# Optimization experiments

Measured on AMD Instinct MI355X. Metric: run time of the kernel, lower is better.

The kernel has to match this reference:

```python
import jax, jax.numpy as jnp
import numpy as np

BATCH = 131072
STATE_DIM = 64
CONTROL_DIM = 16
HIDDEN = 256
ALPHA = 0.1
MAX_ITERS = 200
TOL = 0.01
TRACKED_ITERS = 5
U_MIN, U_MAX = -1.0, 1.0


def setup_inputs() -> dict:
    key = jax.random.key(0)
    ks = jax.random.split(key, 8)
    def w(k, shape, fan_in):
        return (jax.random.normal(k, shape, jnp.float32) / np.float32(np.sqrt(fan_in)))
    x = jax.random.normal(ks[0], (BATCH, STATE_DIM), jnp.float32)
    t = jax.random.uniform(ks[1], (1,), jnp.float32)
    W1 = w(ks[2], (STATE_DIM + 1, HIDDEN), STATE_DIM + 1)
    b1 = jnp.zeros((HIDDEN,), jnp.float32)
    W2 = w(ks[3], (HIDDEN, HIDDEN), HIDDEN)
    b2 = jnp.zeros((HIDDEN,), jnp.float32)
    W3 = w(ks[4], (HIDDEN, STATE_DIM), HIDDEN)
    b3 = jnp.zeros((STATE_DIM,), jnp.float32)
    Bmat = w(ks[5], (STATE_DIM, CONTROL_DIM), STATE_DIM)  # oc_problem dynamics matrix
    return {"x": x, "t": t, "W1": W1, "b1": b1, "W2": W2, "b2": b2,
            "W3": W3, "b3": b3, "Bmat": Bmat}


def _p_net(t, x, W1, b1, W2, b2, W3, b3):
    # DefaultPNet: pad x with scalar t, then 3-layer ReLU MLP -> p in [B, state_dim]
    n = x.shape[0]
    tcol = jnp.broadcast_to(t.reshape(1, 1).astype(x.dtype), (n, 1))
    zt = jnp.concatenate([x, tcol], axis=1)
    h = jax.nn.relu(zt @ W1 + b1)
    h = jax.nn.relu(h @ W2 + b2)
    return h @ W3 + b3


def reference(x, t, W1, b1, W2, b2, W3, b3, Bmat):
    # grad_H_u(t,x,u,p) = u + p @ Bmat  (LQ Hamiltonian); p independent of u,
    # so p is computed once (same math as recomputing it every iteration).
    p = _p_net(t, x, W1, b1, W2, b2, W3, b3)          # [B, state_dim]
    pB = p @ Bmat                                      # [B, control_dim]
    clamp = lambda u: jnp.clip(u, U_MIN, U_MAX)
    T = lambda u, pb: u - ALPHA * (u + pb)

    u0 = jnp.zeros((x.shape[0], CONTROL_DIM), x.dtype)
    pB_ng = jax.lax.stop_gradient(pB)

    def cond(st):
        _, i, res = st
        return (res >= TOL) & (i < MAX_ITERS)

    def body(st):
        u, i, _ = st
        u_new = clamp(T(u, pB_ng))
        res = jnp.max(jnp.linalg.norm(u_new - u, axis=1)) / ALPHA
        return (u_new, i + 1, res)

    u_fp, _, _ = jax.lax.while_loop(cond, body, (u0, jnp.int32(0), jnp.float32(jnp.inf)))

    # training path: tracked_iters differentiable refinement steps + final T
    u = jax.lax.stop_gradient(u_fp)
    for _ in range(TRACKED_ITERS + 1):
        u = clamp(T(u, pB))
    return u
```

## Files before the change

kernel.cpp:

```cpp
#include <hip/hip_runtime.h>


typedef __bf16 bf16;
typedef __bf16 bf16x8 __attribute__((ext_vector_type(8)));
typedef __bf16 bf16x4 __attribute__((ext_vector_type(4)));
typedef float  f32x4  __attribute__((ext_vector_type(4)));

#define HID    256
#define SDIM   64
#define CDIM   16
#define BM     128
#define NTILES 1024
#define GRID   256
#define LDH    264
#define LDX    72

#define OFF_W1P 0
#define OFF_W2P 32768
#define OFF_W3P 163840

#define MFMA(a, b, c) __builtin_amdgcn_mfma_f32_16x16x32_bf16(a, b, c, 0, 0, 0)

__global__ __launch_bounds__(256)
void oc_setup(const float* __restrict__ W1, const float* __restrict__ W2,
              const float* __restrict__ W3, const float* __restrict__ Bmat,
              char* __restrict__ ws) {
  const int gid = blockIdx.x * 256 + threadIdx.x;
  if (gid < 2048) {
    const int f = gid, lane = f & 63, tt = f >> 6;
    const int nt = tt & 15, kt = tt >> 4;
    const int col = nt * 16 + (lane & 15);
    const int krow = kt * 32 + ((lane >> 4) << 3);
    bf16x8 v;
#pragma unroll
    for (int j = 0; j < 8; ++j) v[j] = (bf16)W1[(krow + j) * HID + col];
    *(bf16x8*)((bf16*)(ws + OFF_W1P) + (size_t)f * 8) = v;
  } else if (gid < 10240) {
    const int f = gid - 2048, lane = f & 63, tt = f >> 6;
    const int nt = tt & 15, kt = tt >> 4;
    const int col = nt * 16 + (lane & 15);
    const int krow = kt * 32 + ((lane >> 4) << 3);
    bf16x8 v;
#pragma unroll
    for (int j = 0; j < 8; ++j) v[j] = (bf16)W2[(krow + j) * HID + col];
    *(bf16x8*)((bf16*)(ws + OFF_W2P) + (size_t)f * 8) = v;
  } else if (gid < 10752) {
    const int f = gid - 10240, lane = f & 63, kt = f >> 6;
    const int lrow = lane & 15;
    const int krow = kt * 32 + ((lane >> 4) << 3);
    bf16x8 v;
#pragma unroll
    for (int j = 0; j < 8; ++j) {
      float s = 0.f;
      for (int m = 0; m < SDIM; ++m)
        s = fmaf(W3[(krow + j) * SDIM + m], Bmat[m * CDIM + lrow], s);
      v[j] = (bf16)s;
    }
    *(bf16x8*)((bf16*)(ws + OFF_W3P) + (size_t)f * 8) = v;
  }
}

__global__ __launch_bounds__(512, 2)
void oc_main(const float* __restrict__ x,  const float* __restrict__ t,
             const float* __restrict__ W1, const float* __restrict__ b1,
             const float* __restrict__ b2g, const float* __restrict__ b3,
             const float* __restrict__ Bmat, const char* __restrict__ ws,
             float* __restrict__ out) {
  __shared__ bf16 sH1[BM][LDH];
  __shared__ bf16 sH2[BM][LDH];
  __shared__ bf16 sX [BM][LDX];
  const int tid  = threadIdx.x;
  const int wave = tid >> 6, lane = tid & 63;
  const int quad = lane >> 4, lrow = lane & 15;

  const bf16* W1p = (const bf16*)(ws + OFF_W1P);
  const bf16* W2p = (const bf16*)(ws + OFF_W2P);
  const bf16* W3p = (const bf16*)(ws + OFF_W3P);

  bf16x8 B1[2][2], B2[8][2];
#pragma unroll
  for (int kt = 0; kt < 2; ++kt)
#pragma unroll
    for (int j = 0; j < 2; ++j)
      B1[kt][j] = *(const bf16x8*)(W1p + ((size_t)(kt * 16 + 2 * wave + j) * 64 + lane) * 8);
#pragma unroll
  for (int kt = 0; kt < 8; ++kt)
#pragma unroll
    for (int j = 0; j < 2; ++j)
      B2[kt][j] = *(const bf16x8*)(W2p + ((size_t)(kt * 16 + 2 * wave + j) * 64 + lane) * 8);

  const float tt = t[0];
  float b1e[2], b2r[2];
#pragma unroll
  for (int j = 0; j < 2; ++j) {
    const int c = (2 * wave + j) * 16 + lrow;
    b1e[j] = b1[c] + tt * W1[SDIM * HID + c];
    b2r[j] = b2g[c];
  }
  float b3B = 0.f;
  for (int m = 0; m < SDIM; ++m) b3B = fmaf(b3[m], Bmat[m * CDIM + lrow], b3B);

  auto stage = [&](int tile) {
    const float* xp = x + (size_t)tile * BM * SDIM;
#pragma unroll
    for (int i = 0; i < 4; ++i) {
      const int q = i * 512 + tid;
      const int r = q >> 4, k4 = (q & 15) * 4;
      const float4 v = *(const float4*)(xp + r * SDIM + k4);
      bf16x4 w = {(bf16)v.x, (bf16)v.y, (bf16)v.z, (bf16)v.w};
      *(bf16x4*)(&sX[r][k4]) = w;
    }
  };

  f32x4 acc[8][2];
  int tile = blockIdx.x;
  stage(tile);
  __syncthreads();

  while (true) {
#pragma unroll
    for (int mt = 0; mt < 8; ++mt) {
      acc[mt][0] = (f32x4){0.f, 0.f, 0.f, 0.f};
      acc[mt][1] = (f32x4){0.f, 0.f, 0.f, 0.f};
    }
#pragma unroll
    for (int kt = 0; kt < 2; ++kt)
#pragma unroll
      for (int mt = 0; mt < 8; ++mt) {
        const bf16x8 a = *(const bf16x8*)(&sX[mt * 16 + lrow][kt * 32 + quad * 8]);
        acc[mt][0] = MFMA(a, B1[kt][0], acc[mt][0]);
        acc[mt][1] = MFMA(a, B1[kt][1], acc[mt][1]);
      }
#pragma unroll
    for (int j = 0; j < 2; ++j) {
      const int c = (2 * wave + j) * 16 + lrow;
#pragma unroll
      for (int mt = 0; mt < 8; ++mt)
#pragma unroll
        for (int r = 0; r < 4; ++r)
          sH1[mt * 16 + quad * 4 + r][c] = (bf16)fmaxf(acc[mt][j][r] + b1e[j], 0.f);
    }
    __syncthreads();

#pragma unroll
    for (int mt = 0; mt < 8; ++mt) {
      acc[mt][0] = (f32x4){0.f, 0.f, 0.f, 0.f};
      acc[mt][1] = (f32x4){0.f, 0.f, 0.f, 0.f};
    }
#pragma unroll
    for (int kt = 0; kt < 8; ++kt)
#pragma unroll
      for (int mt = 0; mt < 8; ++mt) {
        const bf16x8 a = *(const bf16x8*)(&sH1[mt * 16 + lrow][kt * 32 + quad * 8]);
        acc[mt][0] = MFMA(a, B2[kt][0], acc[mt][0]);
        acc[mt][1] = MFMA(a, B2[kt][1], acc[mt][1]);
      }
    const int next = tile + GRID;
    if (next < NTILES) stage(next);
    __syncthreads();

#pragma unroll
    for (int j = 0; j < 2; ++j) {
      const int c = (2 * wave + j) * 16 + lrow;
#pragma unroll
      for (int mt = 0; mt < 8; ++mt)
#pragma unroll
        for (int r = 0; r < 4; ++r) {
          const float v = fmaxf(acc[mt][j][r] + b2r[j], 0.f);
          const bf16 hi = (bf16)v;
          sH2[mt * 16 + quad * 4 + r][c] = hi;
          sH1[mt * 16 + quad * 4 + r][c] = (bf16)(v - (float)hi);
        }
    }
    __syncthreads();

    f32x4 a3 = (f32x4){0.f, 0.f, 0.f, 0.f};
#pragma unroll
    for (int kt = 0; kt < 8; ++kt) {
      const bf16x8 b  = *(const bf16x8*)(W3p + ((size_t)(kt * 64) + lane) * 8);
      const bf16x8 ah = *(const bf16x8*)(&sH2[16 * wave + lrow][kt * 32 + quad * 8]);
      const bf16x8 al = *(const bf16x8*)(&sH1[16 * wave + lrow][kt * 32 + quad * 8]);
      a3 = MFMA(ah, b, a3);
      a3 = MFMA(al, b, a3);
    }
    float* op = out + ((size_t)tile * BM + 16 * wave + quad * 4) * CDIM + lrow;
#pragma unroll
    for (int r = 0; r < 4; ++r)
      op[r * CDIM] = fminf(fmaxf(-(a3[r] + b3B), -1.f), 1.f);

    tile = next;
    if (tile >= NTILES) break;
    __syncthreads();
  }
}

extern "C" void kernel_launch(void* const* d_in, const int* in_sizes, int n_in,
                              void* d_out, int out_size, void* d_ws, size_t ws_size,
                              hipStream_t stream) {
  const float* x    = (const float*)d_in[0];
  const float* t    = (const float*)d_in[1];
  const float* W1   = (const float*)d_in[2];
  const float* b1   = (const float*)d_in[3];
  const float* W2   = (const float*)d_in[4];
  const float* b2   = (const float*)d_in[5];
  const float* W3   = (const float*)d_in[6];
  const float* b3   = (const float*)d_in[7];
  const float* Bmat = (const float*)d_in[8];
  float* out = (float*)d_out;
  char*  ws  = (char*)d_ws;

  hipLaunchKernelGGL(oc_setup, dim3(42), dim3(256), 0, stream, W1, W2, W3, Bmat, ws);
  hipLaunchKernelGGL(oc_main, dim3(GRID), dim3(512), 0, stream,
                     x, t, W1, b1, b2, b3, Bmat, ws, out);
}
```

Measured before the change: 130.7 us.

## Fuse weight prep into main kernel, transpose MFMA roles, swizzle shared memory

Drops the separate setup kernel and workspace. Each block now converts W1/W2 to bf16 fragments directly from global memory and computes W3·Bmat into shared memory. The GEMMs are transposed so weights are the A operand and activations the B operand, which allows vectorized bf16x4 stores of hidden activations and float4 output stores. An XOR swizzle on shared-memory hidden buffers reduces bank conflicts. The trade-off is redundant per-block weight conversion with strided, uncoalesced fp32 loads of W1/W2, in exchange for removing one kernel launch.

```diff
diff --git a/kernel.cpp b/kernel.cpp
--- a/kernel.cpp
+++ b/kernel.cpp
@@ -10,186 +10,192 @@
 #define SDIM   64
 #define CDIM   16
 #define BM     128
-#define NTILES 1024
 #define GRID   256
+#define ITERS  4
 #define LDH    264
 #define LDX    72
 
-#define OFF_W1P 0
-#define OFF_W2P 32768
-#define OFF_W3P 163840
-
 #define MFMA(a, b, c) __builtin_amdgcn_mfma_f32_16x16x32_bf16(a, b, c, 0, 0, 0)
 
-__global__ __launch_bounds__(256)
-void oc_setup(const float* __restrict__ W1, const float* __restrict__ W2,
-              const float* __restrict__ W3, const float* __restrict__ Bmat,
-              char* __restrict__ ws) {
-  const int gid = blockIdx.x * 256 + threadIdx.x;
-  if (gid < 2048) {
-    const int f = gid, lane = f & 63, tt = f >> 6;
-    const int nt = tt & 15, kt = tt >> 4;
-    const int col = nt * 16 + (lane & 15);
-    const int krow = kt * 32 + ((lane >> 4) << 3);
-    bf16x8 v;
-#pragma unroll
-    for (int j = 0; j < 8; ++j) v[j] = (bf16)W1[(krow + j) * HID + col];
-    *(bf16x8*)((bf16*)(ws + OFF_W1P) + (size_t)f * 8) = v;
-  } else if (gid < 10240) {
-    const int f = gid - 2048, lane = f & 63, tt = f >> 6;
-    const int nt = tt & 15, kt = tt >> 4;
-    const int col = nt * 16 + (lane & 15);
-    const int krow = kt * 32 + ((lane >> 4) << 3);
-    bf16x8 v;
-#pragma unroll
-    for (int j = 0; j < 8; ++j) v[j] = (bf16)W2[(krow + j) * HID + col];
-    *(bf16x8*)((bf16*)(ws + OFF_W2P) + (size_t)f * 8) = v;
-  } else if (gid < 10752) {
-    const int f = gid - 10240, lane = f & 63, kt = f >> 6;
-    const int lrow = lane & 15;
-    const int krow = kt * 32 + ((lane >> 4) << 3);
-    bf16x8 v;
-#pragma unroll
-    for (int j = 0; j < 8; ++j) {
-      float s = 0.f;
-      for (int m = 0; m < SDIM; ++m)
-        s = fmaf(W3[(krow + j) * SDIM + m], Bmat[m * CDIM + lrow], s);
-      v[j] = (bf16)s;
-    }
-    *(bf16x8*)((bf16*)(ws + OFF_W3P) + (size_t)f * 8) = v;
-  }
+__device__ __forceinline__ int sh_idx(int row, int h) {
+  const int g = (h >> 3) ^ (row & 7);
+  return row * LDH + g * 8 + (h & 7);
 }
 
 __global__ __launch_bounds__(512, 2)
 void oc_main(const float* __restrict__ x,  const float* __restrict__ t,
              const float* __restrict__ W1, const float* __restrict__ b1,
-             const float* __restrict__ b2g, const float* __restrict__ b3,
-             const float* __restrict__ Bmat, const char* __restrict__ ws,
-             float* __restrict__ out) {
-  __shared__ bf16 sH1[BM][LDH];
-  __shared__ bf16 sH2[BM][LDH];
-  __shared__ bf16 sX [BM][LDX];
+             const float* __restrict__ W2, const float* __restrict__ b2,
+             const float* __restrict__ W3, const float* __restrict__ b3,
+             const float* __restrict__ Bmat, float* __restrict__ out) {
+  __shared__ bf16 sH1[BM * LDH];
+  __shared__ bf16 sH2[BM * LDH];
+  __shared__ bf16 sX [BM * LDX];
   const int tid  = threadIdx.x;
   const int wave = tid >> 6, lane = tid & 63;
-  const int quad = lane >> 4, lrow = lane & 15;
-
-  const bf16* W1p = (const bf16*)(ws + OFF_W1P);
-  const bf16* W2p = (const bf16*)(ws + OFF_W2P);
-  const bf16* W3p = (const bf16*)(ws + OFF_W3P);
-
-  bf16x8 B1[2][2], B2[8][2];
-#pragma unroll
-  for (int kt = 0; kt < 2; ++kt)
-#pragma unroll
-    for (int j = 0; j < 2; ++j)
-      B1[kt][j] = *(const bf16x8*)(W1p + ((size_t)(kt * 16 + 2 * wave + j) * 64 + lane) * 8);
-#pragma unroll
-  for (int kt = 0; kt < 8; ++kt)
-#pragma unroll
-    for (int j = 0; j < 2; ++j)
-      B2[kt][j] = *(const bf16x8*)(W2p + ((size_t)(kt * 16 + 2 * wave + j) * 64 + lane) * 8);
-
-  const float tt = t[0];
-  float b1e[2], b2r[2];
-#pragma unroll
-  for (int j = 0; j < 2; ++j) {
-    const int c = (2 * wave + j) * 16 + lrow;
-    b1e[j] = b1[c] + tt * W1[SDIM * HID + c];
-    b2r[j] = b2g[c];
-  }
-  float b3B = 0.f;
-  for (int m = 0; m < SDIM; ++m) b3B = fmaf(b3[m], Bmat[m * CDIM + lrow], b3B);
+  const int q    = lane >> 4, l = lane & 15;
 
   auto stage = [&](int tile) {
     const float* xp = x + (size_t)tile * BM * SDIM;
 #pragma unroll
     for (int i = 0; i < 4; ++i) {
-      const int q = i * 512 + tid;
-      const int r = q >> 4, k4 = (q & 15) * 4;
+      const int e = i * 512 + tid;
+      const int r = e >> 4, k4 = (e & 15) * 4;
       const float4 v = *(const float4*)(xp + r * SDIM + k4);
       bf16x4 w = {(bf16)v.x, (bf16)v.y, (bf16)v.z, (bf16)v.w};
-      *(bf16x4*)(&sX[r][k4]) = w;
+      *(bf16x4*)(&sX[r * LDX + k4]) = w;
     }
   };
 
-  f32x4 acc[8][2];
-  int tile = blockIdx.x;
-  stage(tile);
+  {
+    const int n1 = tid >> 1;
+    const int cb = (tid & 1) * 8;
+    float aw[8];
+#pragma unroll
+    for (int i = 0; i < 8; ++i) aw[i] = 0.f;
+    for (int m = 0; m < SDIM; ++m) {
+      const float w = W3[n1 * SDIM + m];
+      const float4 bA = *(const float4*)(&Bmat[m * CDIM + cb]);
+      const float4 bB = *(const float4*)(&Bmat[m * CDIM + cb + 4]);
+      aw[0] = fmaf(w, bA.x, aw[0]); aw[1] = fmaf(w, bA.y, aw[1]);
+      aw[2] = fmaf(w, bA.z, aw[2]); aw[3] = fmaf(w, bA.w, aw[3]);
+      aw[4] = fmaf(w, bB.x, aw[4]); aw[5] = fmaf(w, bB.y, aw[5]);
+      aw[6] = fmaf(w, bB.z, aw[6]); aw[7] = fmaf(w, bB.w, aw[7]);
+    }
+    const int kt = n1 >> 5, qq = (n1 >> 3) & 3, jj = n1 & 7;
+#pragma unroll
+    for (int ci = 0; ci < 8; ++ci)
+      sH1[(kt * 64 + qq * 16 + cb + ci) * 8 + jj] = (bf16)aw[ci];
+  }
+  stage(blockIdx.x);
   __syncthreads();
 
-  while (true) {
-#pragma unroll
-    for (int mt = 0; mt < 8; ++mt) {
-      acc[mt][0] = (f32x4){0.f, 0.f, 0.f, 0.f};
-      acc[mt][1] = (f32x4){0.f, 0.f, 0.f, 0.f};
-    }
+  bf16x8 W3t[8];
+#pragma unroll
+  for (int kt = 0; kt < 8; ++kt)
+    W3t[kt] = *(const bf16x8*)(&sH1[(kt * 64 + lane) * 8]);
+
+  bf16x8 W1t[2][2], W2t[8][2];
+#pragma unroll
+  for (int kt = 0; kt < 2; ++kt)
+#pragma unroll
+    for (int mt = 0; mt < 2; ++mt) {
+      bf16x8 v;
+#pragma unroll
+      for (int j = 0; j < 8; ++j)
+        v[j] = (bf16)W1[(32 * kt + 8 * q + j) * HID + 32 * wave + 16 * mt + l];
+      W1t[kt][mt] = v;
+    }
+#pragma unroll
+  for (int kt = 0; kt < 8; ++kt)
+#pragma unroll
+    for (int mt = 0; mt < 2; ++mt) {
+      bf16x8 v;
+#pragma unroll
+      for (int j = 0; j < 8; ++j)
+        v[j] = (bf16)W2[(32 * kt + 8 * q + j) * HID + 32 * wave + 16 * mt + l];
+      W2t[kt][mt] = v;
+    }
+
+  const float tt = t[0];
+  f32x4 b1e[2], b2e[2];
+#pragma unroll
+  for (int mt = 0; mt < 2; ++mt)
+#pragma unroll
+    for (int r = 0; r < 4; ++r) {
+      const int h = 32 * wave + 16 * mt + 4 * q + r;
+      b1e[mt][r] = b1[h] + tt * W1[SDIM * HID + h];
+      b2e[mt][r] = b2[h];
+    }
+  f32x4 b3t = (f32x4){0.f, 0.f, 0.f, 0.f};
+  for (int m = 0; m < SDIM; ++m) {
+    const float bm = b3[m];
+    const float4 v = *(const float4*)(&Bmat[m * CDIM + 4 * q]);
+    b3t[0] = fmaf(bm, v.x, b3t[0]); b3t[1] = fmaf(bm, v.y, b3t[1]);
+    b3t[2] = fmaf(bm, v.z, b3t[2]); b3t[3] = fmaf(bm, v.w, b3t[3]);
+  }
+  __syncthreads();
+
+  f32x4 acc[2][8];
+
+  for (int it = 0; it < ITERS; ++it) {
+    const int tile = blockIdx.x + it * GRID;
+
+#pragma unroll
+    for (int mt = 0; mt < 2; ++mt)
+#pragma unroll
+      for (int nt = 0; nt < 8; ++nt) acc[mt][nt] = (f32x4){0.f, 0.f, 0.f, 0.f};
 #pragma unroll
     for (int kt = 0; kt < 2; ++kt)
 #pragma unroll
-      for (int mt = 0; mt < 8; ++mt) {
-        const bf16x8 a = *(const bf16x8*)(&sX[mt * 16 + lrow][kt * 32 + quad * 8]);
-        acc[mt][0] = MFMA(a, B1[kt][0], acc[mt][0]);
-        acc[mt][1] = MFMA(a, B1[kt][1], acc[mt][1]);
-      }
-#pragma unroll
-    for (int j = 0; j < 2; ++j) {
-      const int c = (2 * wave + j) * 16 + lrow;
-#pragma unroll
-      for (int mt = 0; mt < 8; ++mt)
-#pragma unroll
-        for (int r = 0; r < 4; ++r)
-          sH1[mt * 16 + quad * 4 + r][c] = (bf16)fmaxf(acc[mt][j][r] + b1e[j], 0.f);
-    }
-    __syncthreads();
-
-#pragma unroll
-    for (int mt = 0; mt < 8; ++mt) {
-      acc[mt][0] = (f32x4){0.f, 0.f, 0.f, 0.f};
-      acc[mt][1] = (f32x4){0.f, 0.f, 0.f, 0.f};
-    }
+      for (int nt = 0; nt < 8; ++nt) {
+        const bf16x8 b = *(const bf16x8*)(&sX[(16 * nt + l) * LDX + 32 * kt + 8 * q]);
+        acc[0][nt] = MFMA(W1t[kt][0], b, acc[0][nt]);
+        acc[1][nt] = MFMA(W1t[kt][1], b, acc[1][nt]);
+      }
+#pragma unroll
+    for (int mt = 0; mt < 2; ++mt) {
+      const int h0 = 32 * wave + 16 * mt + 4 * q;
+#pragma unroll
+      for (int nt = 0; nt < 8; ++nt) {
+        bf16x4 v;
+#pragma unroll
+        for (int r = 0; r < 4; ++r) v[r] = (bf16)fmaxf(acc[mt][nt][r] + b1e[mt][r], 0.f);
+        *(bf16x4*)(&sH1[sh_idx(16 * nt + l, h0)]) = v;
+      }
+    }
+    __syncthreads();
+
+#pragma unroll
+    for (int mt = 0; mt < 2; ++mt)
+#pragma unroll
+      for (int nt = 0; nt < 8; ++nt) acc[mt][nt] = (f32x4){0.f, 0.f, 0.f, 0.f};
 #pragma unroll
     for (int kt = 0; kt < 8; ++kt)
 #pragma unroll
-      for (int mt = 0; mt < 8; ++mt) {
-        const bf16x8 a = *(const bf16x8*)(&sH1[mt * 16 + lrow][kt * 32 + quad * 8]);
-        acc[mt][0] = MFMA(a, B2[kt][0], acc[mt][0]);
-        acc[mt][1] = MFMA(a, B2[kt][1], acc[mt][1]);
-      }
-    const int next = tile + GRID;
-    if (next < NTILES) stage(next);
-    __syncthreads();
-
-#pragma unroll
-    for (int j = 0; j < 2; ++j) {
-      const int c = (2 * wave + j) * 16 + lrow;
-#pragma unroll
-      for (int mt = 0; mt < 8; ++mt)
+      for (int nt = 0; nt < 8; ++nt) {
+        const bf16x8 b = *(const bf16x8*)(&sH1[sh_idx(16 * nt + l, 32 * kt + 8 * q)]);
+        acc[0][nt] = MFMA(W2t[kt][0], b, acc[0][nt]);
+        acc[1][nt] = MFMA(W2t[kt][1], b, acc[1][nt]);
+      }
+    if (it + 1 < ITERS) stage(tile + GRID);
+    __syncthreads();
+
+#pragma unroll
+    for (int mt = 0; mt < 2; ++mt) {
+      const int h0 = 32 * wave + 16 * mt + 4 * q;
+#pragma unroll
+      for (int nt = 0; nt < 8; ++nt) {
+        bf16x4 hi, lo;
 #pragma unroll
         for (int r = 0; r < 4; ++r) {
-          const float v = fmaxf(acc[mt][j][r] + b2r[j], 0.f);
-          const bf16 hi = (bf16)v;
-          sH2[mt * 16 + quad * 4 + r][c] = hi;
-          sH1[mt * 16 + quad * 4 + r][c] = (bf16)(v - (float)hi);
+          const float v = fmaxf(acc[mt][nt][r] + b2e[mt][r], 0.f);
+          const bf16 h = (bf16)v;
+          hi[r] = h;
+          lo[r] = (bf16)(v - (float)h);
         }
+        const int idx = sh_idx(16 * nt + l, h0);
+        *(bf16x4*)(&sH2[idx]) = hi;
+        *(bf16x4*)(&sH1[idx]) = lo;
+      }
     }
     __syncthreads();
 
     f32x4 a3 = (f32x4){0.f, 0.f, 0.f, 0.f};
 #pragma unroll
     for (int kt = 0; kt < 8; ++kt) {
-      const bf16x8 b  = *(const bf16x8*)(W3p + ((size_t)(kt * 64) + lane) * 8);
-      const bf16x8 ah = *(const bf16x8*)(&sH2[16 * wave + lrow][kt * 32 + quad * 8]);
-      const bf16x8 al = *(const bf16x8*)(&sH1[16 * wave + lrow][kt * 32 + quad * 8]);
-      a3 = MFMA(ah, b, a3);
-      a3 = MFMA(al, b, a3);
-    }
-    float* op = out + ((size_t)tile * BM + 16 * wave + quad * 4) * CDIM + lrow;
+      const int idx = sh_idx(16 * wave + l, 32 * kt + 8 * q);
+      const bf16x8 bh = *(const bf16x8*)(&sH2[idx]);
+      const bf16x8 bl = *(const bf16x8*)(&sH1[idx]);
+      a3 = MFMA(W3t[kt], bh, a3);
+      a3 = MFMA(W3t[kt], bl, a3);
+    }
+    f32x4 o;
 #pragma unroll
     for (int r = 0; r < 4; ++r)
-      op[r * CDIM] = fminf(fmaxf(-(a3[r] + b3B), -1.f), 1.f);
-
-    tile = next;
-    if (tile >= NTILES) break;
+      o[r] = fminf(fmaxf(-(a3[r] + b3t[r]), -1.f), 1.f);
+    *(float4*)(&out[((size_t)tile * BM + 16 * wave + l) * CDIM + 4 * q]) = *(float4*)&o;
+
     __syncthreads();
   }
 }
@@ -207,9 +213,8 @@
   const float* b3   = (const float*)d_in[7];
   const float* Bmat = (const float*)d_in[8];
   float* out = (float*)d_out;
-  char*  ws  = (char*)d_ws;
-
-  hipLaunchKernelGGL(oc_setup, dim3(42), dim3(256), 0, stream, W1, W2, W3, Bmat, ws);
+  (void)d_ws; (void)ws_size;
+
   hipLaunchKernelGGL(oc_main, dim3(GRID), dim3(512), 0, stream,
-                     x, t, W1, b1, b2, b3, Bmat, ws, out);
+                     x, t, W1, b1, W2, b2, W3, b3, Bmat, out);
 }
```

Result: slower. 163.1 us (+24.8%).
